# Kernel tuning notes

Measured on AMD Instinct MI355X. Metric: run time of the kernel, lower is better.

The kernel has to match this reference:

```python
import jax, jax.numpy as jnp
import numpy as np

GH = 256       # GRU hidden size
VOCAB = 1000
MAX_EP = 150
NPREV = NCURR = NNEXT = 64


def _gru_scan(emb, h0, wih, whh, bih, bhh):
    # torch nn.GRU single-layer math, scanned over the token axis
    H = h0.shape[0]
    def step(h, x_t):
        gi = wih @ x_t + bih            # [3H]
        gh = whh @ h + bhh              # [3H]
        r = jax.nn.sigmoid(gi[:H] + gh[:H])
        z = jax.nn.sigmoid(gi[H:2 * H] + gh[H:2 * H])
        n = jnp.tanh(gi[2 * H:] + r * gh[2 * H:])
        hn = (1.0 - z) * n + z * h
        return hn, hn
    _, hs = jax.lax.scan(step, h0, emb)
    return hs                            # [L, H]


def _conv(x, w, b, s):
    y = jax.lax.conv_general_dilated(x, w, (s, s), 'VALID',
                                     dimension_numbers=('NCHW', 'OIHW', 'NCHW'))
    return y + b[None, :, None, None]


def setup_inputs():
    key = jax.random.key(0)
    ks = jax.random.split(key, 48)
    f32 = jnp.float32
    def W(i, shape, s=0.05):
        return (jax.random.normal(ks[i], shape) * s).astype(f32)
    inp = dict(
        x=jax.random.normal(ks[0], (1, 3, 124, 124), f32),
        hx=jax.random.normal(ks[1], (1, 256), f32),
        cx=jax.random.normal(ks[2], (1, 256), f32),
        conv1_w=W(3, (128, 3, 8, 8)), conv1_b=jnp.zeros((128,), f32),
        conv2_w=W(4, (64, 128, 4, 4)), conv2_b=jnp.zeros((64,), f32),
        conv3_w=W(5, (64, 64, 4, 4)), conv3_b=jnp.zeros((64,), f32),
        emb_w=W(6, (VOCAB, 32), 1.0),
        gru_f_wih=W(7, (3 * GH, 32)), gru_f_whh=W(8, (3 * GH, GH)),
        gru_f_bih=jnp.zeros((3 * GH,), f32), gru_f_bhh=jnp.zeros((3 * GH,), f32),
        gru_b_wih=W(9, (3 * GH, 32)), gru_b_whh=W(10, (3 * GH, GH)),
        gru_b_bih=jnp.zeros((3 * GH,), f32), gru_b_bhh=jnp.zeros((3 * GH,), f32),
        time_emb_w=W(11, (MAX_EP + 1, 32), 1.0),
        temp_emb_w=W(12, (2, 32), 1.0),
        img_emb_w=W(13, (256, 64 * 6 * 6)), img_emb_b=jnp.zeros((256,), f32),
        attn_key_w=W(14, (256, 256 * 3)), attn_key_b=jnp.zeros((256,), f32),
        bilinear_A=W(15, (1, 256, 544)), bilinear_b=jnp.zeros((1,), f32),
        reduce_w=W(16, (128, 544)), reduce_b=jnp.zeros((128,), f32),
        gate_w=W(17, (64, 640)), gate_b=jnp.zeros((64,), f32),
        lin_w=W(18, (256, 64 * 6 * 6)), lin_b=jnp.zeros((256,), f32),
        lstm_wih=W(19, (1024, 256)), lstm_whh=W(20, (1024, 256)),
        lstm_bih=jnp.zeros((1024,), f32), lstm_bhh=jnp.zeros((1024,), f32),
        critic_w=W(21, (1, 288)), critic_b=jnp.zeros((1,), f32),
        actor_w=W(22, (4, 288)), actor_b=jnp.zeros((4,), f32),
        prev_inst=jax.random.randint(ks[23], (1, NPREV), 0, VOCAB),
        curr_inst=jax.random.randint(ks[24], (1, NCURR), 0, VOCAB),
        next_inst=jax.random.randint(ks[25], (1, NNEXT), 0, VOCAB),
        tx=jax.random.randint(ks[26], (1,), 0, MAX_EP + 1),
    )
    return inp


def reference(x, hx, cx, conv1_w, conv1_b, conv2_w, conv2_b, conv3_w, conv3_b,
              emb_w, gru_f_wih, gru_f_whh, gru_f_bih, gru_f_bhh,
              gru_b_wih, gru_b_whh, gru_b_bih, gru_b_bhh,
              time_emb_w, temp_emb_w, img_emb_w, img_emb_b,
              attn_key_w, attn_key_b, bilinear_A, bilinear_b,
              reduce_w, reduce_b, gate_w, gate_b, lin_w, lin_b,
              lstm_wih, lstm_whh, lstm_bih, lstm_bhh,
              critic_w, critic_b, actor_w, actor_b,
              prev_inst, curr_inst, next_inst, tx):
    np_, nc, nn_ = prev_inst.shape[1], curr_inst.shape[1], next_inst.shape[1]
    all_inst = jnp.concatenate([prev_inst, curr_inst, next_inst], axis=1)[0]  # [L]
    L = all_inst.shape[0]

    # CNN encoder
    h = jax.nn.relu(_conv(x, conv1_w, conv1_b, 4))
    h = jax.nn.relu(_conv(h, conv2_w, conv2_b, 2))
    x_img = jax.nn.relu(_conv(h, conv3_w, conv3_b, 2))       # [1,64,6,6]

    # token-looped GRUs -> single lax.scan each (note: original runs gru_b
    # over the SAME forward order then reverses the hidden list; replicated)
    emb = emb_w[all_inst]                                    # [L,32]
    h0 = jnp.zeros((GH,), emb.dtype)
    hs_f = _gru_scan(emb, h0, gru_f_wih, gru_f_whh, gru_f_bih, gru_f_bhh)
    hs_b = _gru_scan(emb, h0, gru_b_wih, gru_b_whh, gru_b_bih, gru_b_bhh)[::-1]
    curr_instr_rep = jnp.concatenate([hs_f[np_ + nc - 1], hs_b[np_]])[None]  # [1,512]
    ir_f = jnp.concatenate([hs_f[:np_], hs_f[L - nn_:]], axis=0)             # [M,256]
    ir_b = jnp.concatenate([hs_b[:np_], hs_b[L - nn_:]], axis=0)
    temp_tok = jnp.concatenate([jnp.zeros((np_,), jnp.int32), jnp.ones((nn_,), jnp.int32)])
    instr_rep = jnp.concatenate([ir_f, ir_b, temp_emb_w[temp_tok]], axis=1)  # [M,544]

    # bilinear attention over prev/next token states
    image_emb = x_img.reshape(1, -1) @ img_emb_w.T + img_emb_b               # [1,256]
    attn_key = jnp.concatenate([curr_instr_rep, image_emb], 1) @ attn_key_w.T + attn_key_b
    scores = jnp.einsum('k,okv,mv->mo', attn_key[0], bilinear_A, instr_rep) + bilinear_b  # [M,1]
    w = jax.nn.softmax(scores, axis=0)
    instr_sum = (instr_rep * w).sum(0, keepdims=True)                        # [1,544]

    # gating of image features
    gating = instr_sum @ reduce_w.T + reduce_b                               # [1,128]
    gate_key = jax.nn.sigmoid(jnp.concatenate([curr_instr_rep, gating], 1) @ gate_w.T + gate_b)  # [1,64]
    xg = (x_img * gate_key[:, :, None, None]).reshape(1, -1)
    z = jax.nn.relu(xg @ lin_w.T + lin_b)                                    # [1,256]

    # LSTMCell (torch gate order i,f,g,o)
    gates = z @ lstm_wih.T + lstm_bih + hx @ lstm_whh.T + lstm_bhh           # [1,1024]
    i, f, g, o = jnp.split(gates, 4, axis=1)
    cx2 = jax.nn.sigmoid(f) * cx + jax.nn.sigmoid(i) * jnp.tanh(g)
    hx2 = jax.nn.sigmoid(o) * jnp.tanh(cx2)

    feat = jnp.concatenate([hx2, time_emb_w[tx].reshape(-1, 32)], axis=1)    # [1,288]
    critic = feat @ critic_w.T + critic_b                                    # [1,1]
    actor = feat @ actor_w.T + actor_b                                       # [1,4]
    return critic, actor, hx2, cx2
```

## Files before the change

kernel.cpp:

```cpp
#include <hip/hip_runtime.h>
#include <hip/hip_bf16.h>

typedef int int4v __attribute__((ext_vector_type(4)));

#define GBLK 130
#define TBLK 128

__device__ __forceinline__ float bf2f(unsigned short u) {
    unsigned int v = ((unsigned int)u) << 16;
    return __builtin_bit_cast(float, v);
}
__device__ __forceinline__ float sigm(float x) { return 1.0f / (1.0f + expf(-x)); }
__device__ __forceinline__ float san(float v) {
    return (v == v && fabsf(v) < 1e20f) ? v : 12345.0f;
}
__device__ __forceinline__ void wrout(void* out, int i, float v, int f32out) {
    if (f32out) ((float*)out)[i] = v;
    else ((__hip_bfloat16*)out)[i] = __float2bfloat16(v);
}
__device__ __forceinline__ float fexp2(float x) {
#if __has_builtin(__builtin_amdgcn_exp2f)
    return __builtin_amdgcn_exp2f(x);
#else
    return exp2f(x);
#endif
}
__device__ __forceinline__ float frcp(float x) {
#if __has_builtin(__builtin_amdgcn_rcpf)
    return __builtin_amdgcn_rcpf(x);
#else
    return 1.0f / x;
#endif
}
__device__ __forceinline__ float fsigm(float x) {
    return frcp(1.0f + fexp2(x * -1.44269504f));
}
__device__ __forceinline__ float ftanh(float x) {
    float t = fexp2(x * 2.88539008f);
    return 1.0f - 2.0f * frcp(t + 1.0f);
}
__device__ __forceinline__ float wave_red(float acc) {
#pragma unroll
    for (int off = 32; off >= 1; off >>= 1) acc += __shfl_down(acc, off);
    return acc;
}
__device__ __forceinline__ int sel4(int4v v, int rg) {
    int a = (rg & 1) ? v.y : v.x;
    int b = (rg & 1) ? v.w : v.z;
    return (rg & 2) ? b : a;
}

__device__ __forceinline__ float ldf(const void* p, int i, int f32) {
    return f32 ? ((const float*)p)[i] : bf2f(((const unsigned short*)p)[i]);
}
__device__ __forceinline__ float2 ldf2(const void* p, int i, int f32) {
    if (f32) return *(const float2*)((const float*)p + i);
    unsigned int u = *(const unsigned int*)((const unsigned short*)p + i);
    return make_float2(bf2f((unsigned short)(u & 0xffff)), bf2f((unsigned short)(u >> 16)));
}
__device__ __forceinline__ float4 ldf4(const void* p, int i, int f32) {
    if (f32) return *(const float4*)((const float*)p + i);
    uint2 u = *(const uint2*)((const unsigned short*)p + i);
    return make_float4(bf2f((unsigned short)(u.x & 0xffff)), bf2f((unsigned short)(u.x >> 16)),
                       bf2f((unsigned short)(u.y & 0xffff)), bf2f((unsigned short)(u.y >> 16)));
}

__device__ __forceinline__ void ast(float* p, float v) {
    __hip_atomic_store(p, v, __ATOMIC_RELAXED, __HIP_MEMORY_SCOPE_AGENT);
}
__device__ __forceinline__ float ald(const float* p) {
    return __hip_atomic_load(p, __ATOMIC_RELAXED, __HIP_MEMORY_SCOPE_AGENT);
}
__device__ __forceinline__ unsigned int aldu(const unsigned int* p) {
    return __hip_atomic_load(p, __ATOMIC_RELAXED, __HIP_MEMORY_SCOPE_AGENT);
}

__device__ __forceinline__ void gbar(unsigned int* bar, unsigned int target) {
    __syncthreads();
    if (threadIdx.x == 0) {
        __threadfence();
        atomicAdd(bar, 1u);
        while (aldu(bar) < target) __builtin_amdgcn_s_sleep(2);
        __threadfence();
    }
    __syncthreads();
}
__device__ __forceinline__ void lbar(unsigned int* bar, unsigned int target) {
    __syncthreads();
    if (threadIdx.x == 0) {
        asm volatile("s_waitcnt vmcnt(0)" ::: "memory");
        atomicAdd(bar, 1u);
        while (aldu(bar) < target) __builtin_amdgcn_s_sleep(1);
    }
    __syncthreads();
    asm volatile("" ::: "memory");
}
__device__ __forceinline__ void sig_release(unsigned int* bar) {
    __syncthreads();
    if (threadIdx.x == 0) {
        __threadfence();
        atomicAdd(bar, 1u);
    }
    __syncthreads();
}
__device__ __forceinline__ void sig_acquire(unsigned int* bar, unsigned int target) {
    __syncthreads();
    if (threadIdx.x == 0) {
        while (aldu(bar) < target) __builtin_amdgcn_s_sleep(2);
        __threadfence();
    }
    __syncthreads();
}
__device__ __forceinline__ void sig_acquire_slow(unsigned int* bar, unsigned int target) {
    __syncthreads();
    if (threadIdx.x == 0) {
        while (aldu(bar) < target) __builtin_amdgcn_s_sleep(64);
        __threadfence();
    }
    __syncthreads();
}

struct CanonArgs {
    const void* ptr[40];
    int start[41];
    int size[40];
};

struct AllArgs {
    CanonArgs ca;
    const void* x; int nx;
    const int* prev; const int* curr; const int* nxt; const int* tx;
    float* ws;
    int T;
    void* out;
};

__global__ void k_flag1000(void* out) {
    if (threadIdx.x == 0) ((unsigned int*)out)[0] = 0x447A0000u;
}

__device__ __forceinline__ float ir_val(int m, int v, const float* hsf, const float* hsb,
                                        const float* temp_emb) {
    if (v < 256) { int r = (m < 64) ? m : 64 + m; return hsf[r * 256 + v]; }
    if (v < 512) { int r = (m < 64) ? 191 - m : 127 - m; return hsb[r * 256 + v - 256]; }
    return temp_emb[(m >= 64) * 32 + (v - 512)];
}

__global__ __launch_bounds__(512, 1) void k_all(AllArgs a) {
    __shared__ float SL[2432];
    const int B = blockIdx.x;
    const int tid = threadIdx.x;
    const int lane = tid & 63;
    const int w = tid >> 6;

    float* ws = a.ws;
    unsigned int* bars = (unsigned int*)(ws + 32);
    float* C = ws + 640;
    const int T = a.T;
    float* gi = C + T;
    float* hs = gi + 294912;
    float* h1 = hs + 98304;
    float* xh2 = h1 + 115200;
    float* ximg = xh2 + 12544;
    float* aux = ximg + 2304;
    float* ak    = aux;
    float* tmpv  = aux + 256;
    float* gk    = aux + 800;
    float* zv    = aux + 864;
    float* sg    = aux + 1120;
    float* sscg  = aux + 2144;
    float* ssumg = aux + 2272;
    float* sgatg = aux + 2816;

#define CP(i) (C + a.ca.start[i])

    float f32in;
    int i64;
    {
        const unsigned short* xs = (const unsigned short*)a.x;
        float mx = 0.0f;
        for (int i = tid; i < a.nx; i += 512) {
            float f = bf2f(xs[i]);
            float v = (f == f) ? fabsf(f) : 1e30f;
            mx = fmaxf(mx, v);
        }
        SL[tid] = mx;
        __syncthreads();
        for (int s = 256; s >= 1; s >>= 1) {
            if (tid < s) SL[tid] = fmaxf(SL[tid], SL[tid + s]);
            __syncthreads();
        }
        f32in = (SL[0] > 100.0f) ? 1.0f : 0.0f;
        int anyOdd = 0;
        for (int k = 0; k < 32; ++k) anyOdd |= a.curr[2 * k + 1];
        i64 = (anyOdd == 0) ? 1 : 0;
        __syncthreads();
    }
    const int tstride = i64 ? 2 : 1;
    const int f32 = (f32in != 0.0f);

    if (B < 2) {
        unsigned int* hq = (unsigned int*)SL;
        float* sc = SL + 128;

        const void* whh_raw = B ? a.ca.ptr[15] : a.ca.ptr[11];
        const void* bhh_raw = B ? a.ca.ptr[17] : a.ca.ptr[13];
        const float* gib = gi + B * 192 * 768;
        float* hso = hs + B * 192 * 256;

        int l = tid & 63;
        int wv = tid >> 6;
        int lg = l >> 4;
        int lr = l & 15;
        int e_sel = (l >> 2) & 1;
        int rg = l & 3;
        int j = 32 * wv + 16 * e_sel + 4 * lg + rg;

        int4v A[3][2][4];
#pragma unroll
        for (int s3 = 0; s3 < 3; ++s3) {
#pragma unroll
            for (int e = 0; e < 2; ++e) {
                int r = s3 * 256 + 32 * wv + 16 * e + lr;
                int rowb = r * 256;
                float4 tmp[16];
                float mx = 0.0f;
#pragma unroll
                for (int q = 0; q < 4; ++q) {
#pragma unroll
                    for (int f = 0; f < 4; ++f) {
                        float4 v = ldf4(whh_raw, rowb + 64 * q + 16 * lg + 4 * f, f32);
                        tmp[q * 4 + f] = v;
                        mx = fmaxf(mx, fmaxf(fmaxf(fabsf(v.x), fabsf(v.y)),
                                             fmaxf(fabsf(v.z), fabsf(v.w))));
                    }
                }
                mx = fmaxf(mx, __shfl_xor(mx, 16));
                mx = fmaxf(mx, __shfl_xor(mx, 32));
                float scale = 127.0f / fmaxf(mx, 1e-20f);
                if (lg == 0) sc[r] = mx * (1.0f / (127.0f * 127.0f));
#pragma unroll
                for (int q = 0; q < 4; ++q) {
                    int dw[4];
#pragma unroll
                    for (int f = 0; f < 4; ++f) {
                        float4 v = tmp[q * 4 + f];
                        int p0 = (int)rintf(v.x * scale) & 0xff;
                        int p1 = (int)rintf(v.y * scale) & 0xff;
                        int p2 = (int)rintf(v.z * scale) & 0xff;
                        int p3 = (int)rintf(v.w * scale);
                        dw[f] = p0 | (p1 << 8) | (p2 << 16) | (p3 << 24);
                    }
                    A[s3][e][q] = (int4v){dw[0], dw[1], dw[2], dw[3]};
                }
            }
        }
        if (tid < 128) hq[tid] = 0u;

        float bhhn = ldf(bhh_raw, 512 + j, f32);
        float invR = 0.0f, invZ = 0.0f, invN = 0.0f;
        sig_acquire(&bars[1], TBLK);
        invR = sc[j];
        invZ = sc[256 + j];
        invN = sc[512 + j];
        int wr8 = ((l & 8) == 0);

        float hprev = 0.0f;
        float cr0 = gib[j],       cz0 = gib[256 + j],  cn0 = gib[512 + j];
        float cr1 = gib[768 + j], cz1 = gib[1024 + j], cn1 = gib[1280 + j];

        int4v zero4 = (int4v){0, 0, 0, 0};

        auto step = [&](const unsigned int* hbuf, unsigned int* hnxt, int S,
                        float gr, float gz, float gn) {
            const char* hb = (const char*)hbuf;
            int4v B0 = *(const int4v*)(hb + 16 * lg);
            int4v B1 = *(const int4v*)(hb + 64 + 16 * lg);
            int4v B2 = *(const int4v*)(hb + 128 + 16 * lg);
            int4v B3 = *(const int4v*)(hb + 192 + 16 * lg);

            int4v C00, C01, C10, C11, C20, C21;
            asm volatile(
                "v_mfma_i32_16x16x64_i8 %0, %7,  %31, %6\n\t"
                "v_mfma_i32_16x16x64_i8 %1, %11, %31, %6\n\t"
                "v_mfma_i32_16x16x64_i8 %2, %15, %31, %6\n\t"
                "v_mfma_i32_16x16x64_i8 %3, %19, %31, %6\n\t"
                "v_mfma_i32_16x16x64_i8 %4, %23, %31, %6\n\t"
                "v_mfma_i32_16x16x64_i8 %5, %27, %31, %6\n\t"
                "v_mfma_i32_16x16x64_i8 %0, %8,  %32, %0\n\t"
                "v_mfma_i32_16x16x64_i8 %1, %12, %32, %1\n\t"
                "v_mfma_i32_16x16x64_i8 %2, %16, %32, %2\n\t"
                "v_mfma_i32_16x16x64_i8 %3, %20, %32, %3\n\t"
                "v_mfma_i32_16x16x64_i8 %4, %24, %32, %4\n\t"
                "v_mfma_i32_16x16x64_i8 %5, %28, %32, %5\n\t"
                "v_mfma_i32_16x16x64_i8 %0, %9,  %33, %0\n\t"
                "v_mfma_i32_16x16x64_i8 %1, %13, %33, %1\n\t"
                "v_mfma_i32_16x16x64_i8 %2, %17, %33, %2\n\t"
                "v_mfma_i32_16x16x64_i8 %3, %21, %33, %3\n\t"
                "v_mfma_i32_16x16x64_i8 %4, %25, %33, %4\n\t"
                "v_mfma_i32_16x16x64_i8 %5, %29, %33, %5\n\t"
                "v_mfma_i32_16x16x64_i8 %0, %10, %34, %0\n\t"
                "v_mfma_i32_16x16x64_i8 %1, %14, %34, %1\n\t"
                "v_mfma_i32_16x16x64_i8 %2, %18, %34, %2\n\t"
                "v_mfma_i32_16x16x64_i8 %3, %22, %34, %3\n\t"
                "v_mfma_i32_16x16x64_i8 %4, %26, %34, %4\n\t"
                "v_mfma_i32_16x16x64_i8 %5, %30, %34, %5\n\t"
                "s_nop 7\n\t"
                "s_nop 7"
                : "=&v"(C00), "=&v"(C01), "=&v"(C10),
                  "=&v"(C11), "=&v"(C20), "=&v"(C21)
                : "v"(zero4),
                  "v"(A[0][0][0]), "v"(A[0][0][1]), "v"(A[0][0][2]), "v"(A[0][0][3]),
                  "v"(A[0][1][0]), "v"(A[0][1][1]), "v"(A[0][1][2]), "v"(A[0][1][3]),
                  "v"(A[1][0][0]), "v"(A[1][0][1]), "v"(A[1][0][2]), "v"(A[1][0][3]),
                  "v"(A[1][1][0]), "v"(A[1][1][1]), "v"(A[1][1][2]), "v"(A[1][1][3]),
                  "v"(A[2][0][0]), "v"(A[2][0][1]), "v"(A[2][0][2]), "v"(A[2][0][3]),
                  "v"(A[2][1][0]), "v"(A[2][1][1]), "v"(A[2][1][2]), "v"(A[2][1][3]),
                  "v"(B0), "v"(B1), "v"(B2), "v"(B3));
            __builtin_amdgcn_sched_barrier(0);

            int ri = sel4(e_sel ? C01 : C00, rg);
            int zi = sel4(e_sel ? C11 : C10, rg);
            int ni = sel4(e_sel ? C21 : C20, rg);
            float ar = (float)ri * invR;
            float az = (float)zi * invZ;
            float an = (float)ni * invN;
            float r = fsigm(gr + ar);
            float z = fsigm(gz + az);
            float n = ftanh(gn + r * (an + bhhn));
            hprev = z * (hprev - n) + n;

            int qv = (int)rintf(hprev * 127.0f);
            if (wr8) {
                hso[S * 256 + j] = hprev;
                ((char*)hnxt)[j] = (char)qv;
            }
            asm volatile("s_waitcnt lgkmcnt(0)" ::: "memory");
            __builtin_amdgcn_s_barrier();
        };

        for (int i = 0; i < 96; ++i) {
            int s0 = 2 * i;
            float nr0 = 0.0f, nz0 = 0.0f, nn0 = 0.0f;
            if (s0 + 2 < 192) {
                const float* gp = gib + (s0 + 2) * 768 + j;
                nr0 = gp[0]; nz0 = gp[256]; nn0 = gp[512];
            }
            step(hq, hq + 64, s0, cr0, cz0, cn0);

            int s1 = s0 + 1;
            float nr1 = 0.0f, nz1 = 0.0f, nn1 = 0.0f;
            if (s1 + 2 < 192) {
                const float* gp = gib + (s1 + 2) * 768 + j;
                nr1 = gp[0]; nz1 = gp[256]; nn1 = gp[512];
            }
            step(hq + 64, hq, s1, cr1, cz1, cn1);

            cr0 = nr0; cz0 = nz0; cn0 = nn0;
            cr1 = nr1; cz1 = nz1; cn1 = nn1;
        }
        sig_release(&bars[2]);
        return;
    }

    const int cb = B - 2;
    const int cw = cb * 8 + w;

    {
        const void* emb  = a.ca.ptr[9];
        const void* wihf = a.ca.ptr[10];
        const void* bihf = a.ca.ptr[12];
        const void* bhhf = a.ca.ptr[13];
        const void* wihb = a.ca.ptr[14];
        const void* bihb = a.ca.ptr[16];
        const void* bhhb = a.ca.ptr[17];
        for (int idx = cb * 512 + tid; idx < 294912; idx += TBLK * 512) {
            int gru = idx / 147456;
            int r = idx - gru * 147456;
            int tt = r / 768;
            int j = r - tt * 768;
            const int* src = (tt < 64) ? a.prev : ((tt < 128) ? a.curr : a.nxt);
            int ti = (tt < 64) ? tt : ((tt < 128) ? tt - 64 : tt - 128);
            int tok = min(max(src[ti * tstride], 0), 999);
            const void* wih = gru ? wihb : wihf;
            const void* bih = gru ? bihb : bihf;
            const void* bhh = gru ? bhhb : bhhf;
            float acc = ldf(bih, j, f32) + ((j < 512) ? ldf(bhh, j, f32) : 0.0f);
#pragma unroll
            for (int k = 0; k < 16; ++k) {
                float2 wv = ldf2(wih, j * 32 + 2 * k, f32);
                float2 ev = ldf2(emb, tok * 32 + 2 * k, f32);
                acc += wv.x * ev.x + wv.y * ev.y;
            }
            gi[idx] = acc;
        }
    }
    sig_release(&bars[1]);

    {
        int nch = T >> 10;
        int g = tid >> 8;
        int l256 = tid & 255;
        for (int ch = cb * 2 + g; ch < nch; ch += 2 * TBLK) {
            int base = ch << 10;
            int t = 0;
            while (t < 39 && base >= a.ca.start[t + 1]) ++t;
            int local = base - a.ca.start[t] + (l256 << 2);
            int sz = a.ca.size[t];
            float4 v = make_float4(0.0f, 0.0f, 0.0f, 0.0f);
            if (local + 3 < sz) {
                v = ldf4(a.ca.ptr[t], local, f32);
            } else if (local < sz) {
                float tmp[4] = {0.0f, 0.0f, 0.0f, 0.0f};
                for (int q = 0; q < 4 && local + q < sz; ++q)
                    tmp[q] = ldf(a.ca.ptr[t], local + q, f32);
                v = make_float4(tmp[0], tmp[1], tmp[2], tmp[3]);
            }
            *(float4*)(C + base + (l256 << 2)) = v;
        }
    }
    gbar(&bars[0], TBLK);

    {
        const float* x = CP(0);
        const float* cw1 = CP(3);
        const float* cb1 = CP(4);
        for (int idx = cb * 512 + tid; idx < 115200; idx += TBLK * 512) {
            int oc = idx / 900;
            int rem = idx - oc * 900;
            int oh = rem / 30;
            int ow = rem - oh * 30;
            float acc = cb1[oc];
            for (int ic = 0; ic < 3; ++ic) {
                int xb = ic * 15376 + (oh * 4) * 124 + ow * 4;
                int wb = oc * 192 + ic * 64;
#pragma unroll
                for (int kh = 0; kh < 8; ++kh) {
                    const float2* xr = (const float2*)(x + xb + kh * 124);
                    const float2* wr = (const float2*)(cw1 + wb + kh * 8);
#pragma unroll
                    for (int p = 0; p < 4; ++p) {
                        float2 xv = xr[p];
                        float2 wv = wr[p];
                        acc += xv.x * wv.x + xv.y * wv.y;
                    }
                }
            }
            h1[idx] = fmaxf(acc, 0.0f);
        }
    }
    gbar(&bars[3], TBLK);

    {
        const float* w2 = CP(5);
        const float* b2 = CP(6);
        for (int wid = cw; wid < 12544; wid += TBLK * 8) {
            int oc = wid / 196;
            int rem = wid - oc * 196;
            int oh = rem / 14, ow = rem - oh * 14;
            float acc = 0.0f;
#pragma unroll 8
            for (int i = 0; i < 32; ++i) {
                int e = lane + (i << 6);
                int ic = e >> 4, k = e & 15, kh = k >> 2, kw = k & 3;
                acc += h1[ic * 900 + (oh * 2 + kh) * 30 + ow * 2 + kw] * w2[oc * 2048 + e];
            }
            acc = wave_red(acc);
            if (lane == 0) xh2[wid] = fmaxf(acc + b2[oc], 0.0f);
        }
    }
    gbar(&bars[4], TBLK);

    {
        const float* w3 = CP(7);
        const float* b3 = CP(8);
        for (int wid = cw; wid < 2304; wid += TBLK * 8) {
            int oc = wid / 36;
            int rem = wid - oc * 36;
            int oh = rem / 6, ow = rem - oh * 6;
            float acc = 0.0f;
#pragma unroll
            for (int i = 0; i < 16; ++i) {
                int e = lane + (i << 6);
                int ic = e >> 4, k = e & 15, kh = k >> 2, kw = k & 3;
                acc += xh2[ic * 196 + (oh * 2 + kh) * 14 + ow * 2 + kw] * w3[oc * 1024 + e];
            }
            acc = wave_red(acc);
            if (lane == 0) ximg[wid] = fmaxf(acc + b3[oc], 0.0f);
        }
    }
    gbar(&bars[5], TBLK);

    {
        const float* iw = CP(20);
        const float* ib = CP(21);
        if (cw < 256) {
            const float* wr = iw + cw * 2304;
            float acc = 0.0f;
            for (int k = lane; k < 2304; k += 64) acc += wr[k] * ximg[k];
            acc = wave_red(acc);
            if (lane == 0) ws[320 + cw] = acc + ib[cw];
        }
    }
    gbar(&bars[6], TBLK);
    sig_acquire_slow(&bars[2], 2u);

    const float* imgemb = ws + 320;
    const float* hsf = hs;
    const float* hsb = hs + 192 * 256;
    const float* temp = CP(19);

    if (cb < 32) {
        if (tid < 256) {
            SL[tid] = hsf[127 * 256 + tid];
            SL[256 + tid] = hsb[127 * 256 + tid];
            SL[512 + tid] = imgemb[tid];
        }
        __syncthreads();
        const float* wr = CP(22) + cw * 768;
        float acc = 0.0f;
        for (int k = lane; k < 768; k += 64) acc += wr[k] * SL[k];
        acc = wave_red(acc);
        if (lane == 0) ast(ak + cw, acc + CP(23)[cw]);
    }
    lbar(&bars[8], TBLK);

    if (cb < 68) {
        if (tid < 256) SL[tid] = ald(ak + tid);
        __syncthreads();
        const float* bA = CP(24);
        float acc = 0.0f;
#pragma unroll
        for (int k = lane; k < 256; k += 64) acc += bA[k * 544 + cw] * SL[k];
        acc = wave_red(acc);
        if (lane == 0) ast(tmpv + cw, acc);
    }
    lbar(&bars[9], TBLK);

    if (cb == 0) {
        float* stmp = SL;
        float* ssc  = SL + 544;
        float* sred = SL + 672;
        for (int v = tid; v < 544; v += 512) stmp[v] = ald(tmpv + v);
        __syncthreads();
        {
            int m = tid >> 2, q = tid & 3;
            float acc = 0.0f;
            for (int v = q * 136; v < q * 136 + 136; ++v)
                acc += stmp[v] * ir_val(m, v, hsf, hsb, temp);
            sred[tid] = acc;
        }
        __syncthreads();
        if (tid < 128) {
            float acc = CP(25)[0];
            for (int q = 0; q < 4; ++q) acc += sred[tid * 4 + q];
            ssc[tid] = acc;
            sred[tid] = acc;
        }
        __syncthreads();
#pragma unroll
        for (int s2 = 64; s2 >= 1; s2 >>= 1) {
            if (tid < s2) sred[tid] = fmaxf(sred[tid], sred[tid + s2]);
            __syncthreads();
        }
        float mx = sred[0];
        __syncthreads();
        if (tid < 128) {
            float e = expf(ssc[tid] - mx);
            ssc[tid] = e;
            sred[tid] = e;
        }
        __syncthreads();
#pragma unroll
        for (int s2 = 64; s2 >= 1; s2 >>= 1) {
            if (tid < s2) sred[tid] += sred[tid + s2];
            __syncthreads();
        }
        float inv = 1.0f / sred[0];
        __syncthreads();
        if (tid < 128) ast(sscg + tid, ssc[tid] * inv);
    }
    lbar(&bars[10], TBLK);

    if (cb < 68) {
        if (tid < 128) SL[tid] = ald(sscg + tid);
        __syncthreads();
        int v = cw;
        float s0 = SL[lane];
        float s1 = SL[lane + 64];
        float acc = s0 * ir_val(lane, v, hsf, hsb, temp) +
                    s1 * ir_val(lane + 64, v, hsf, hsb, temp);
        acc = wave_red(acc);
        if (lane == 0) ast(ssumg + v, acc);
    }
    lbar(&bars[11], TBLK);

    if (cb < 16) {
        for (int v = tid; v < 544; v += 512) SL[v] = ald(ssumg + v);
        __syncthreads();
        int jr = cw;
        const float* wr = CP(26) + jr * 544;
        float acc = 0.0f;
        for (int k = lane; k < 544; k += 64) acc += wr[k] * SL[k];
        acc = wave_red(acc);
        if (lane == 0) ast(sgatg + jr, acc + CP(27)[jr]);
    }
    lbar(&bars[12], TBLK);

    if (cb < 8) {
        if (tid < 256) {
            SL[tid] = hsf[127 * 256 + tid];
            SL[256 + tid] = hsb[127 * 256 + tid];
        }
        if (tid < 128) SL[512 + tid] = ald(sgatg + tid);
        __syncthreads();
        int jr = cw;
        const float* wr = CP(28) + jr * 640;
        float acc = 0.0f;
        for (int k = lane; k < 640; k += 64) acc += wr[k] * SL[k];
        acc = wave_red(acc);
        if (lane == 0) ast(gk + jr, sigm(acc + CP(29)[jr]));
    }
    lbar(&bars[13], TBLK);

    if (cb < 32) {
        if (tid < 64) SL[tid] = ald(gk + tid);
        __syncthreads();
        const float* wr = CP(30) + cw * 2304;
        float acc = 0.0f;
        for (int k = lane; k < 2304; k += 64) acc += wr[k] * ximg[k] * SL[k / 36];
        acc = wave_red(acc);
        if (lane == 0) ast(zv + cw, fmaxf(acc + CP(31)[cw], 0.0f));
    }
    lbar(&bars[14], TBLK);

    {
        if (tid < 256) SL[tid] = ald(zv + tid);
        __syncthreads();
        const float* wi = CP(32) + cw * 256;
        const float* wh = CP(33) + cw * 256;
        const float* hx = CP(1);
        float acc = 0.0f;
#pragma unroll
        for (int k = lane; k < 256; k += 64) acc += wi[k] * SL[k] + wh[k] * hx[k];
        acc = wave_red(acc);
        if (lane == 0) ast(sg + cw, acc + CP(34)[cw] + CP(35)[cw]);
    }
    lbar(&bars[15], TBLK);

    if (cb == 0) {
        const float* cx = CP(2);
        float* sfeat = SL;
        float* sh2   = SL + 320;
        float* sc2   = SL + 576;
        float* stmp  = SL + 832;
        float* sred  = SL + 1344;

        if (tid < 256) {
            float ii = ald(sg + tid), ff = ald(sg + 256 + tid);
            float gg = ald(sg + 512 + tid), oo = ald(sg + 768 + tid);
            float c2 = sigm(ff) * cx[tid] + sigm(ii) * tanhf(gg);
            float h2 = sigm(oo) * tanhf(c2);
            sc2[tid] = c2;
            sh2[tid] = h2;
            sfeat[tid] = h2;
        }
        if (tid < 32) {
            int t192 = min(max(a.tx[0], 0), 150);
            sfeat[256 + tid] = CP(18)[t192 * 32 + tid];
        }
        __syncthreads();

        stmp[tid] = (tid < 288) ? CP(36)[tid] * sfeat[tid] : 0.0f;
        {
            const float* acw = CP(38);
            int aa = tid >> 7, k = tid & 127;
            float pa = acw[aa * 288 + k] * sfeat[k] +
                       acw[aa * 288 + 128 + k] * sfeat[128 + k];
            if (k < 32) pa += acw[aa * 288 + 256 + k] * sfeat[256 + k];
            sred[tid] = pa;
        }
        __syncthreads();
#pragma unroll
        for (int s2 = 256; s2 >= 1; s2 >>= 1) {
            if (tid < s2) stmp[tid] += stmp[tid + s2];
            int k = tid & 127;
            if (s2 <= 64 && k < s2) sred[tid] += sred[tid + s2];
            __syncthreads();
        }

        if (tid == 0) wrout(a.out, 0, san(stmp[0] + CP(37)[0]), f32);
        if (tid < 4) wrout(a.out, 1 + tid, san(sred[tid * 128] + CP(39)[tid]), f32);
        if (tid < 256) {
            wrout(a.out, 5 + tid, san(sh2[tid]), f32);
            wrout(a.out, 261 + tid, san(sc2[tid]), f32);
        }
    }
#undef CP
}

extern "C" void kernel_launch(void* const* d_in, const int* in_sizes, int n_in,
                              void* d_out, int out_size, void* d_ws, size_t ws_size,
                              hipStream_t stream) {
    if (n_in != 44) return;

    AllArgs aa;
    int acc = 0;
    for (int i = 0; i < 40; ++i) {
        aa.ca.ptr[i] = d_in[i];
        aa.ca.start[i] = acc;
        aa.ca.size[i] = in_sizes[i];
        acc += (in_sizes[i] + 1023) & ~1023;
    }
    aa.ca.start[40] = acc;
    const int T = acc;

    size_t need = (size_t)(640 + T + 294912 + 98304 + 115200 + 12544 + 2304 + 2944) * 4;
    if (ws_size < need) {
        k_flag1000<<<1, 64, 0, stream>>>(d_out);
        return;
    }

    aa.x = d_in[0];
    aa.nx = in_sizes[0];
    aa.prev = (const int*)d_in[40];
    aa.curr = (const int*)d_in[41];
    aa.nxt  = (const int*)d_in[42];
    aa.tx   = (const int*)d_in[43];
    aa.ws = (float*)d_ws;
    aa.T = T;
    aa.out = d_out;

    hipMemsetAsync((char*)d_ws + 128, 0, 64, stream);
    k_all<<<GBLK, 512, 0, stream>>>(aa);
}
```

Measured before the change: 433.0 us.

## Offload GRU weight quantization to worker blocks and pipeline input-projection chunks

The int8 quantization of the GRU recurrent weights moves from the two scan blocks to the 128 worker blocks, which write quantized rows and scales to workspace. The scan blocks wait on a new flag and then load the packed weights directly. The input-gate precompute is split into four time chunks, each with its own release flag, so the recurrence can start before all projections finish. Worker blocks also touch later-stage weights to warm the cache while waiting for the scan. The cost is more barriers and workspace, plus an extra global round trip for the quantized weights.

```diff
diff --git a/kernel.cpp b/kernel.cpp
--- a/kernel.cpp
+++ b/kernel.cpp
@@ -43,6 +43,11 @@
 #pragma unroll
     for (int off = 32; off >= 1; off >>= 1) acc += __shfl_down(acc, off);
     return acc;
+}
+__device__ __forceinline__ float wave_max(float m) {
+#pragma unroll
+    for (int off = 32; off >= 1; off >>= 1) m = fmaxf(m, __shfl_down(m, off));
+    return __shfl(m, 0);
 }
 __device__ __forceinline__ int sel4(int4v v, int rg) {
     int a = (rg & 1) ? v.y : v.x;
@@ -171,39 +176,35 @@
     float* sscg  = aux + 2144;
     float* ssumg = aux + 2272;
     float* sgatg = aux + 2816;
+    int*   wq8   = (int*)(aux + 2944);
+    float* scg   = aux + 2944 + 98304;
 
 #define CP(i) (C + a.ca.start[i])
 
-    float f32in;
-    int i64;
-    {
-        const unsigned short* xs = (const unsigned short*)a.x;
-        float mx = 0.0f;
-        for (int i = tid; i < a.nx; i += 512) {
-            float f = bf2f(xs[i]);
-            float v = (f == f) ? fabsf(f) : 1e30f;
-            mx = fmaxf(mx, v);
-        }
-        SL[tid] = mx;
-        __syncthreads();
-        for (int s = 256; s >= 1; s >>= 1) {
-            if (tid < s) SL[tid] = fmaxf(SL[tid], SL[tid + s]);
+    if (B < 2) {
+        float f32in;
+        {
+            const unsigned short* xs = (const unsigned short*)a.x;
+            float mx = 0.0f;
+            for (int i = tid; i < a.nx; i += 512) {
+                float f = bf2f(xs[i]);
+                float v = (f == f) ? fabsf(f) : 1e30f;
+                mx = fmaxf(mx, v);
+            }
+            SL[tid] = mx;
             __syncthreads();
-        }
-        f32in = (SL[0] > 100.0f) ? 1.0f : 0.0f;
-        int anyOdd = 0;
-        for (int k = 0; k < 32; ++k) anyOdd |= a.curr[2 * k + 1];
-        i64 = (anyOdd == 0) ? 1 : 0;
-        __syncthreads();
-    }
-    const int tstride = i64 ? 2 : 1;
-    const int f32 = (f32in != 0.0f);
-
-    if (B < 2) {
+            for (int s = 256; s >= 1; s >>= 1) {
+                if (tid < s) SL[tid] = fmaxf(SL[tid], SL[tid + s]);
+                __syncthreads();
+            }
+            f32in = SL[0];
+            __syncthreads();
+        }
+        const int f32 = (f32in > 100.0f);
+
         unsigned int* hq = (unsigned int*)SL;
-        float* sc = SL + 128;
-
-        const void* whh_raw = B ? a.ca.ptr[15] : a.ca.ptr[11];
+        if (tid < 128) hq[tid] = 0u;
+
         const void* bhh_raw = B ? a.ca.ptr[17] : a.ca.ptr[13];
         const float* gib = gi + B * 192 * 768;
         float* hso = hs + B * 192 * 256;
@@ -216,54 +217,27 @@
         int rg = l & 3;
         int j = 32 * wv + 16 * e_sel + 4 * lg + rg;
 
+        sig_acquire(&bars[6], TBLK);
         int4v A[3][2][4];
 #pragma unroll
         for (int s3 = 0; s3 < 3; ++s3) {
 #pragma unroll
             for (int e = 0; e < 2; ++e) {
                 int r = s3 * 256 + 32 * wv + 16 * e + lr;
-                int rowb = r * 256;
-                float4 tmp[16];
-                float mx = 0.0f;
-#pragma unroll
-                for (int q = 0; q < 4; ++q) {
-#pragma unroll
-                    for (int f = 0; f < 4; ++f) {
-                        float4 v = ldf4(whh_raw, rowb + 64 * q + 16 * lg + 4 * f, f32);
-                        tmp[q * 4 + f] = v;
-                        mx = fmaxf(mx, fmaxf(fmaxf(fabsf(v.x), fabsf(v.y)),
-                                             fmaxf(fabsf(v.z), fabsf(v.w))));
-                    }
-                }
-                mx = fmaxf(mx, __shfl_xor(mx, 16));
-                mx = fmaxf(mx, __shfl_xor(mx, 32));
-                float scale = 127.0f / fmaxf(mx, 1e-20f);
-                if (lg == 0) sc[r] = mx * (1.0f / (127.0f * 127.0f));
-#pragma unroll
-                for (int q = 0; q < 4; ++q) {
-                    int dw[4];
-#pragma unroll
-                    for (int f = 0; f < 4; ++f) {
-                        float4 v = tmp[q * 4 + f];
-                        int p0 = (int)rintf(v.x * scale) & 0xff;
-                        int p1 = (int)rintf(v.y * scale) & 0xff;
-                        int p2 = (int)rintf(v.z * scale) & 0xff;
-                        int p3 = (int)rintf(v.w * scale);
-                        dw[f] = p0 | (p1 << 8) | (p2 << 16) | (p3 << 24);
-                    }
-                    A[s3][e][q] = (int4v){dw[0], dw[1], dw[2], dw[3]};
-                }
-            }
-        }
-        if (tid < 128) hq[tid] = 0u;
-
+                const int4v* src = (const int4v*)(wq8 + (B * 768 + r) * 64 + lg * 16);
+                A[s3][e][0] = src[0];
+                A[s3][e][1] = src[1];
+                A[s3][e][2] = src[2];
+                A[s3][e][3] = src[3];
+            }
+        }
+        float invR = scg[B * 768 + j];
+        float invZ = scg[B * 768 + 256 + j];
+        float invN = scg[B * 768 + 512 + j];
         float bhhn = ldf(bhh_raw, 512 + j, f32);
-        float invR = 0.0f, invZ = 0.0f, invN = 0.0f;
+        int wr8 = ((l & 8) == 0);
+
         sig_acquire(&bars[1], TBLK);
-        invR = sc[j];
-        invZ = sc[256 + j];
-        invN = sc[512 + j];
-        int wr8 = ((l & 8) == 0);
 
         float hprev = 0.0f;
         float cr0 = gib[j],       cz0 = gib[256 + j],  cn0 = gib[512 + j];
@@ -340,6 +314,9 @@
         };
 
         for (int i = 0; i < 96; ++i) {
+            if (i == 23) sig_acquire(&bars[2], TBLK);
+            if (i == 47) sig_acquire(&bars[3], TBLK);
+            if (i == 71) sig_acquire(&bars[4], TBLK);
             int s0 = 2 * i;
             float nr0 = 0.0f, nz0 = 0.0f, nn0 = 0.0f;
             if (s0 + 2 < 192) {
@@ -359,12 +336,55 @@
             cr0 = nr0; cz0 = nz0; cn0 = nn0;
             cr1 = nr1; cz1 = nz1; cn1 = nn1;
         }
-        sig_release(&bars[2]);
+        sig_release(&bars[5]);
         return;
     }
 
     const int cb = B - 2;
     const int cw = cb * 8 + w;
+
+    float f32in;
+    int i64;
+    {
+        const unsigned short* xs = (const unsigned short*)a.x;
+        float mx = 0.0f;
+        for (int i = tid; i < a.nx; i += 512) {
+            float f = bf2f(xs[i]);
+            float v = (f == f) ? fabsf(f) : 1e30f;
+            mx = fmaxf(mx, v);
+        }
+        SL[tid] = mx;
+        __syncthreads();
+        for (int s = 256; s >= 1; s >>= 1) {
+            if (tid < s) SL[tid] = fmaxf(SL[tid], SL[tid + s]);
+            __syncthreads();
+        }
+        f32in = SL[0];
+        int anyOdd = 0;
+        for (int k = 0; k < 32; ++k) anyOdd |= a.curr[2 * k + 1];
+        i64 = (anyOdd == 0) ? 1 : 0;
+        __syncthreads();
+    }
+    const int tstride = i64 ? 2 : 1;
+    const int f32 = (f32in > 100.0f);
+
+    {
+        for (int r2 = cw; r2 < 1536; r2 += 1024) {
+            int dir = r2 / 768, row = r2 - dir * 768;
+            const void* raw = dir ? a.ca.ptr[15] : a.ca.ptr[11];
+            float4 v = ldf4(raw, row * 256 + lane * 4, f32);
+            float m = fmaxf(fmaxf(fabsf(v.x), fabsf(v.y)), fmaxf(fabsf(v.z), fabsf(v.w)));
+            m = wave_max(m);
+            float scale = 127.0f / fmaxf(m, 1e-20f);
+            int p0 = (int)rintf(v.x * scale) & 0xff;
+            int p1 = (int)rintf(v.y * scale) & 0xff;
+            int p2 = (int)rintf(v.z * scale) & 0xff;
+            int p3 = (int)rintf(v.w * scale);
+            wq8[(dir * 768 + row) * 64 + lane] = p0 | (p1 << 8) | (p2 << 16) | (p3 << 24);
+            if (lane == 0) scg[dir * 768 + row] = m * (1.0f / (127.0f * 127.0f));
+        }
+    }
+    sig_release(&bars[6]);
 
     {
         const void* emb  = a.ca.ptr[9];
@@ -374,28 +394,30 @@
         const void* wihb = a.ca.ptr[14];
         const void* bihb = a.ca.ptr[16];
         const void* bhhb = a.ca.ptr[17];
-        for (int idx = cb * 512 + tid; idx < 294912; idx += TBLK * 512) {
-            int gru = idx / 147456;
-            int r = idx - gru * 147456;
-            int tt = r / 768;
-            int j = r - tt * 768;
-            const int* src = (tt < 64) ? a.prev : ((tt < 128) ? a.curr : a.nxt);
-            int ti = (tt < 64) ? tt : ((tt < 128) ? tt - 64 : tt - 128);
-            int tok = min(max(src[ti * tstride], 0), 999);
-            const void* wih = gru ? wihb : wihf;
-            const void* bih = gru ? bihb : bihf;
-            const void* bhh = gru ? bhhb : bhhf;
-            float acc = ldf(bih, j, f32) + ((j < 512) ? ldf(bhh, j, f32) : 0.0f);
-#pragma unroll
-            for (int k = 0; k < 16; ++k) {
-                float2 wv = ldf2(wih, j * 32 + 2 * k, f32);
-                float2 ev = ldf2(emb, tok * 32 + 2 * k, f32);
-                acc += wv.x * ev.x + wv.y * ev.y;
-            }
-            gi[idx] = acc;
-        }
-    }
-    sig_release(&bars[1]);
+        for (int c = 0; c < 4; ++c) {
+            for (int li = cb * 512 + tid; li < 73728; li += TBLK * 512) {
+                int gru = li / 36864;
+                int rr = li - gru * 36864;
+                int tt = c * 48 + rr / 768;
+                int j = rr - (rr / 768) * 768;
+                const int* src = (tt < 64) ? a.prev : ((tt < 128) ? a.curr : a.nxt);
+                int ti = (tt < 64) ? tt : ((tt < 128) ? tt - 64 : tt - 128);
+                int tok = min(max(src[ti * tstride], 0), 999);
+                const void* wih = gru ? wihb : wihf;
+                const void* bih = gru ? bihb : bihf;
+                const void* bhh = gru ? bhhb : bhhf;
+                float acc = ldf(bih, j, f32) + ((j < 512) ? ldf(bhh, j, f32) : 0.0f);
+#pragma unroll
+                for (int k = 0; k < 16; ++k) {
+                    float2 wv = ldf2(wih, j * 32 + 2 * k, f32);
+                    float2 ev = ldf2(emb, tok * 32 + 2 * k, f32);
+                    acc += wv.x * ev.x + wv.y * ev.y;
+                }
+                gi[(gru * 192 + tt) * 768 + j] = acc;
+            }
+            sig_release(&bars[1 + c]);
+        }
+    }
 
     {
         int nch = T >> 10;
@@ -449,7 +471,7 @@
             h1[idx] = fmaxf(acc, 0.0f);
         }
     }
-    gbar(&bars[3], TBLK);
+    gbar(&bars[7], TBLK);
 
     {
         const float* w2 = CP(5);
@@ -469,7 +491,7 @@
             if (lane == 0) xh2[wid] = fmaxf(acc + b2[oc], 0.0f);
         }
     }
-    gbar(&bars[4], TBLK);
+    gbar(&bars[8], TBLK);
 
     {
         const float* w3 = CP(7);
@@ -489,7 +511,7 @@
             if (lane == 0) ximg[wid] = fmaxf(acc + b3[oc], 0.0f);
         }
     }
-    gbar(&bars[5], TBLK);
+    gbar(&bars[9], TBLK);
 
     {
         const float* iw = CP(20);
@@ -499,11 +521,41 @@
             float acc = 0.0f;
             for (int k = lane; k < 2304; k += 64) acc += wr[k] * ximg[k];
             acc = wave_red(acc);
-            if (lane == 0) ws[320 + cw] = acc + ib[cw];
-        }
-    }
-    gbar(&bars[6], TBLK);
-    sig_acquire_slow(&bars[2], 2u);
+            if (lane == 0) ast(ws + 320 + cw, acc + ib[cw]);
+        }
+    }
+    lbar(&bars[10], TBLK);
+
+    {
+        float pf = 0.0f;
+        if (cb < 32) {
+            const float* wr = CP(22) + cw * 768;
+            for (int k = lane; k < 768; k += 64) pf += wr[k];
+            const float* lr2 = CP(30) + cw * 2304;
+            for (int k = lane; k < 2304; k += 64) pf += lr2[k];
+        }
+        if (cb < 68) {
+            const float* bA = CP(24);
+#pragma unroll
+            for (int k = lane; k < 256; k += 64) pf += bA[k * 544 + cw];
+        }
+        if (cb < 16) {
+            const float* wr = CP(26) + cw * 544;
+            for (int k = lane; k < 544; k += 64) pf += wr[k];
+        }
+        if (cb < 8) {
+            const float* wr = CP(28) + cw * 640;
+            for (int k = lane; k < 640; k += 64) pf += wr[k];
+        }
+        {
+            const float* wi = CP(32) + cw * 256;
+            const float* wh = CP(33) + cw * 256;
+#pragma unroll
+            for (int k = lane; k < 256; k += 64) pf += wi[k] + wh[k];
+        }
+        asm volatile("" :: "v"(pf));
+    }
+    sig_acquire_slow(&bars[5], 2u);
 
     const float* imgemb = ws + 320;
     const float* hsf = hs;
@@ -514,7 +566,7 @@
         if (tid < 256) {
             SL[tid] = hsf[127 * 256 + tid];
             SL[256 + tid] = hsb[127 * 256 + tid];
-            SL[512 + tid] = imgemb[tid];
+            SL[512 + tid] = ald(imgemb + tid);
         }
         __syncthreads();
         const float* wr = CP(22) + cw * 768;
@@ -523,7 +575,7 @@
         acc = wave_red(acc);
         if (lane == 0) ast(ak + cw, acc + CP(23)[cw]);
     }
-    lbar(&bars[8], TBLK);
+    lbar(&bars[11], TBLK);
 
     if (cb < 68) {
         if (tid < 256) SL[tid] = ald(ak + tid);
@@ -535,7 +587,7 @@
         acc = wave_red(acc);
         if (lane == 0) ast(tmpv + cw, acc);
     }
-    lbar(&bars[9], TBLK);
+    lbar(&bars[12], TBLK);
 
     if (cb == 0) {
         float* stmp = SL;
@@ -580,7 +632,7 @@
         __syncthreads();
         if (tid < 128) ast(sscg + tid, ssc[tid] * inv);
     }
-    lbar(&bars[10], TBLK);
+    lbar(&bars[13], TBLK);
 
     if (cb < 68) {
         if (tid < 128) SL[tid] = ald(sscg + tid);
@@ -593,7 +645,7 @@
         acc = wave_red(acc);
         if (lane == 0) ast(ssumg + v, acc);
     }
-    lbar(&bars[11], TBLK);
+    lbar(&bars[14], TBLK);
 
     if (cb < 16) {
         for (int v = tid; v < 544; v += 512) SL[v] = ald(ssumg + v);
@@ -605,7 +657,7 @@
         acc = wave_red(acc);
         if (lane == 0) ast(sgatg + jr, acc + CP(27)[jr]);
     }
-    lbar(&bars[12], TBLK);
+    lbar(&bars[15], TBLK);
 
     if (cb < 8) {
         if (tid < 256) {
@@ -621,7 +673,7 @@
         acc = wave_red(acc);
         if (lane == 0) ast(gk + jr, sigm(acc + CP(29)[jr]));
     }
-    lbar(&bars[13], TBLK);
+    lbar(&bars[16], TBLK);
 
     if (cb < 32) {
         if (tid < 64) SL[tid] = ald(gk + tid);
@@ -632,7 +684,7 @@
         acc = wave_red(acc);
         if (lane == 0) ast(zv + cw, fmaxf(acc + CP(31)[cw], 0.0f));
     }
-    lbar(&bars[14], TBLK);
+    lbar(&bars[17], TBLK);
 
     {
         if (tid < 256) SL[tid] = ald(zv + tid);
@@ -646,7 +698,7 @@
         acc = wave_red(acc);
         if (lane == 0) ast(sg + cw, acc + CP(34)[cw] + CP(35)[cw]);
     }
-    lbar(&bars[15], TBLK);
+    lbar(&bars[18], TBLK);
 
     if (cb == 0) {
         const float* cx = CP(2);
@@ -715,7 +767,8 @@
     aa.ca.start[40] = acc;
     const int T = acc;
 
-    size_t need = (size_t)(640 + T + 294912 + 98304 + 115200 + 12544 + 2304 + 2944) * 4;
+    size_t need = (size_t)(640 + T + 294912 + 98304 + 115200 + 12544 + 2304 +
+                           2944 + 98304 + 1536) * 4;
     if (ws_size < need) {
         k_flag1000<<<1, 64, 0, stream>>>(d_out);
         return;
@@ -731,6 +784,6 @@
     aa.T = T;
     aa.out = d_out;
 
-    hipMemsetAsync((char*)d_ws + 128, 0, 64, stream);
+    hipMemsetAsync((char*)d_ws + 128, 0, 96, stream);
     k_all<<<GBLK, 512, 0, stream>>>(aa);
 }
```

Measured after the change: 439.8 us. Within noise of the previous version (+1.6%).
